# Kernel tuning notes

Hardware: AMD Instinct MI355X
Metric: run time of the kernel (lower is better)

The kernel has to match this reference:

```python
import jax, jax.numpy as jnp
import numpy as np

B, T, D_MODEL, D_FF, NUM_EXPERTS, TOP_K = 8, 4096, 512, 2048, 8, 2
VOCAB = 50257


def setup_inputs() -> dict:
    key = jax.random.key(0)
    k_x, k_id, k_w1, k_w2 = jax.random.split(key, 4)
    x = jax.random.normal(k_x, (B, T, D_MODEL), dtype=jnp.float32)
    token_ids = jax.random.randint(k_id, (B, T), 0, VOCAB, dtype=jnp.int32)
    # stacked expert MLP params: Linear(D,F) -> GELU -> Linear(F,D)
    W1 = jax.random.normal(k_w1, (NUM_EXPERTS, D_MODEL, D_FF), dtype=jnp.float32) * 0.02
    b1 = jnp.zeros((NUM_EXPERTS, D_FF), dtype=jnp.float32)
    W2 = jax.random.normal(k_w2, (NUM_EXPERTS, D_FF, D_MODEL), dtype=jnp.float32) * 0.02
    b2 = jnp.zeros((NUM_EXPERTS, D_MODEL), dtype=jnp.float32)
    return {"x": x, "token_ids": token_ids, "W1": W1, "b1": b1, "W2": W2, "b2": b2}


def reference(x, token_ids, W1, b1, W2, b2):
    Bx, Tx, D = x.shape
    E = W1.shape[0]
    top_k = TOP_K
    # hash routing: expert_ids[b,t,k] = (b*T + token_ids[b,t] + k) % E
    rows = (jnp.arange(Bx, dtype=jnp.int32) * Tx)[:, None, None]           # (B,1,1)
    offs = jnp.arange(top_k, dtype=jnp.int32)                               # (K,)
    expert_ids = (rows + token_ids[:, :, None] + offs) % E                  # (B,T,K)
    onehot = jax.nn.one_hot(expert_ids, E, dtype=jnp.float32)               # (B,T,K,E)
    hits = onehot.sum(axis=2)                                               # (B,T,E) hit counts
    # per-hit combine weight in torch source: (1/top_k)/top_k = 1/top_k^2
    comb_w = hits / float(top_k * top_k)
    # masked-dense expert MLP == dense MLP on x with output masked (per-token ops)
    out = jnp.zeros_like(x)
    for e in range(E):  # fixed small loop over experts
        h = jax.nn.gelu(x @ W1[e] + b1[e], approximate=False)               # (B,T,F)
        y = h @ W2[e] + b2[e]                                               # (B,T,D)
        out = out + y * comb_w[..., e:e + 1]
    expert_counts = hits.sum(axis=(0, 1))                                   # (E,)
    return out, expert_ids, expert_counts
```

## Files before the change

### kernel.cpp

```cpp
#include <hip/hip_runtime.h>
#include <math.h>

#define NUM_E 8
#define NTOK  32768
#define TSEQ  4096
#define DM    512
#define DF    2048
#define CAP   6144

typedef unsigned short ushort_t;
typedef __attribute__((ext_vector_type(8))) short short8;
typedef __attribute__((ext_vector_type(4))) float floatx4;

__device__ __forceinline__ unsigned short f2bf(float f){
  union { float f; unsigned int u; } v; v.f = f;
  unsigned int u = v.u;
  unsigned int r = (u + 0x7FFFu + ((u >> 16) & 1u)) >> 16;
  return (unsigned short)r;
}

__device__ __forceinline__ float gelu_fast(float h){
  float z = h * (1.5957691216057308f + 0.0713548162726009f * h * h);
  float e = __expf(-z);
  return h * __builtin_amdgcn_rcpf(1.0f + e);
}

__device__ __forceinline__ void gld_lds16(const void* g, void* l){
  __builtin_amdgcn_global_load_lds(
      (const __attribute__((address_space(1))) unsigned int*)g,
      (__attribute__((address_space(3))) unsigned int*)l, 16, 0, 0);
}

__global__ void k_init(int* cnt){
  if (threadIdx.x < NUM_E) cnt[threadIdx.x] = 0;
}

__global__ __launch_bounds__(1024) void k_route(
    const int* __restrict__ tok, float* __restrict__ ids_out,
    int* __restrict__ cnt, int* __restrict__ list){
  __shared__ int lcnt[NUM_E];
  __shared__ int lbase[NUM_E];
  int tid = threadIdx.x;
  if (tid < NUM_E) lcnt[tid] = 0;
  __syncthreads();
  int flat = blockIdx.x * 1024 + tid;
  int b = flat >> 12;
  int t = tok[flat];
  int base = b * TSEQ + t;
  int e0 = base & 7;
  int e1 = (base + 1) & 7;
  ids_out[2*flat]   = (float)e0;
  ids_out[2*flat+1] = (float)e1;
  int lpos = atomicAdd(&lcnt[e0], 1);
  __syncthreads();
  if (tid < NUM_E) lbase[tid] = atomicAdd(&cnt[tid], lcnt[tid]);
  __syncthreads();
  int pos = lbase[e0] + lpos;
  if (pos < CAP) list[e0*CAP + pos] = flat;
}

__global__ void k_finalize(const int* __restrict__ cnt, int* __restrict__ off,
                           float* __restrict__ counts_out){
  int tid = threadIdx.x;
  if (tid == 0){
    int s = 0;
    for (int c = 0; c < NUM_E; c++){ off[c] = s; s += cnt[c]; }
    off[NUM_E] = s;
  }
  if (tid < NUM_E)
    counts_out[tid] = (float)(cnt[tid] + cnt[(tid + 7) & 7]);
}

__global__ void k_convert_x(const float* __restrict__ x, ushort_t* __restrict__ xb){
  int i = blockIdx.x * blockDim.x + threadIdx.x;
  float4 v = ((const float4*)x)[i];
  ushort4 o;
  o.x = f2bf(v.x); o.y = f2bf(v.y); o.z = f2bf(v.z); o.w = f2bf(v.w);
  ((ushort4*)xb)[i] = o;
}

__global__ void k_transpose_cvt(const float* __restrict__ in, ushort_t* __restrict__ out,
                                int R, int C){
  __shared__ ushort_t s[64][65];
  int e = blockIdx.z;
  int c0 = blockIdx.x * 64, r0 = blockIdx.y * 64;
  const float* ine = in + (size_t)e * R * C;
  ushort_t* oute = out + (size_t)e * R * C;
  int tx = threadIdx.x & 63, ty = threadIdx.x >> 6;
  for (int rr = ty; rr < 64; rr += 4)
    s[rr][tx] = f2bf(ine[(size_t)(r0+rr)*C + c0 + tx]);
  __syncthreads();
  for (int cc = ty; cc < 64; cc += 4)
    oute[(size_t)(c0+cc)*R + r0 + tx] = s[tx][cc];
}


__global__ __launch_bounds__(256, 4) void k_gemm1(
    const ushort_t* __restrict__ xb, const ushort_t* __restrict__ w1t,
    const float* __restrict__ b1,
    const int* __restrict__ cnt, const int* __restrict__ off,
    const int* __restrict__ list, ushort_t* __restrict__ H, int c0)
{
  int c = c0 + (blockIdx.z >> 1), slot = blockIdx.z & 1;
  int e = (c + slot) & 7;
  int n_c = cnt[c];
  int m0 = blockIdx.x * 128;
  if (m0 >= n_c) return;
  int n0 = blockIdx.y * 128;

  __shared__ alignas(16) ushort_t As[128*64];
  __shared__ alignas(16) ushort_t Bs[128*64];
  __shared__ unsigned int rowoff[128];

  int tid = threadIdx.x;
  int lane = tid & 63, w = tid >> 6;

  if (tid < 128){
    int i = m0 + tid;
    int tk = list[c*CAP + ((i < n_c) ? i : 0)];
    rowoff[tid] = (unsigned int)tk * (DM*2);
  }
  __syncthreads();

  int rl = lane >> 3;
  int cc = (lane & 7) ^ rl;
  unsigned int aoff[4], boff[4];
  const char* w1te = (const char*)w1t + (size_t)e * ((size_t)DF*DM*2);
  #pragma unroll
  for (int j = 0; j < 4; j++){
    int r = j*32 + w*8 + rl;
    aoff[j] = rowoff[r] + (unsigned int)cc*16u;
    boff[j] = (unsigned int)(n0 + r) * (DM*2) + (unsigned int)cc*16u;
  }

  floatx4 acc[4][4];
  #pragma unroll
  for (int a = 0; a < 4; a++)
    #pragma unroll
    for (int q = 0; q < 4; q++) acc[a][q] = floatx4{0.f,0.f,0.f,0.f};

  int wr = w >> 1, wc = w & 1;
  int col = lane & 15, quad = lane >> 4;
  int xa = col & 7;
  const ushort_t* A0 = As + (wr*64 + col)*64 + (quad ^ xa)*8;
  const ushort_t* A1 = As + (wr*64 + col)*64 + ((quad + 4) ^ xa)*8;
  const ushort_t* B0 = Bs + (wc*64 + col)*64 + (quad ^ xa)*8;
  const ushort_t* B1 = Bs + (wc*64 + col)*64 + ((quad + 4) ^ xa)*8;
  char* AsW = (char*)As + w*1024;
  char* BsW = (char*)Bs + w*1024;

  for (int k0 = 0; k0 < DM; k0 += 64){
    #pragma unroll
    for (int j = 0; j < 4; j++){
      gld_lds16((const char*)xb + aoff[j] + k0*2, AsW + j*4096);
      gld_lds16(w1te + boff[j] + k0*2, BsW + j*4096);
    }
    __syncthreads();
    {
      short8 a[4], bfr[4];
      #pragma unroll
      for (int mi = 0; mi < 4; mi++) a[mi] = *(const short8*)(A0 + mi*1024);
      #pragma unroll
      for (int ni = 0; ni < 4; ni++) bfr[ni] = *(const short8*)(B0 + ni*1024);
      #pragma unroll
      for (int mi = 0; mi < 4; mi++)
        #pragma unroll
        for (int ni = 0; ni < 4; ni++)
          acc[mi][ni] = __builtin_amdgcn_mfma_f32_16x16x32_bf16(a[mi], bfr[ni], acc[mi][ni], 0, 0, 0);
      #pragma unroll
      for (int mi = 0; mi < 4; mi++) a[mi] = *(const short8*)(A1 + mi*1024);
      #pragma unroll
      for (int ni = 0; ni < 4; ni++) bfr[ni] = *(const short8*)(B1 + ni*1024);
      #pragma unroll
      for (int mi = 0; mi < 4; mi++)
        #pragma unroll
        for (int ni = 0; ni < 4; ni++)
          acc[mi][ni] = __builtin_amdgcn_mfma_f32_16x16x32_bf16(a[mi], bfr[ni], acc[mi][ni], 0, 0, 0);
    }
    __syncthreads();
  }

  int hbase = off[c] - off[c0];
  const float* b1e = b1 + e*DF;
  #pragma unroll
  for (int mi = 0; mi < 4; mi++){
    #pragma unroll
    for (int r = 0; r < 4; r++){
      int m = wr*64 + mi*16 + quad*4 + r;
      int i = m0 + m;
      if (i < n_c){
        size_t hrow = (size_t)(hbase + i)*(2*DF) + (size_t)slot*DF + n0 + wc*64;
        #pragma unroll
        for (int ni = 0; ni < 4; ni++){
          int nl = ni*16 + col;
          float v = acc[mi][ni][r] + b1e[n0 + wc*64 + nl];
          H[hrow + nl] = f2bf(gelu_fast(v));
        }
      }
    }
  }
}

__global__ __launch_bounds__(256, 4) void k_gemm2(
    const ushort_t* __restrict__ H, const ushort_t* __restrict__ w2t,
    const float* __restrict__ b2,
    const int* __restrict__ cnt, const int* __restrict__ off,
    const int* __restrict__ list, float* __restrict__ out, int c0, int nb)
{
  int c = c0 + blockIdx.z;
  int e1 = (c + 1) & 7;
  int n_c = cnt[c];
  int m0 = blockIdx.x * 128;
  if (m0 >= n_c) return;
  int n0 = blockIdx.y * 128;

  __shared__ alignas(16) ushort_t As[128*64];
  __shared__ alignas(16) ushort_t Bs[128*64];
  __shared__ int rowtok[128];

  int tid = threadIdx.x;
  int lane = tid & 63, w = tid >> 6;
  int rowbase = off[c] - off[c0];
  int phaseTok = off[c0 + nb] - off[c0];

  if (tid < 128){
    int i = m0 + tid;
    rowtok[tid] = list[c*CAP + ((i < n_c) ? i : 0)];
  }

  int rl = lane >> 3;
  int cc = (lane & 7) ^ rl;
  unsigned int aoff[4], boff[4];
  #pragma unroll
  for (int j = 0; j < 4; j++){
    int r = j*32 + w*8 + rl;
    int rg = rowbase + m0 + r;
    if (rg > phaseTok - 1) rg = phaseTok - 1;
    aoff[j] = (unsigned int)rg * (2*DF*2) + (unsigned int)cc*16u;
    boff[j] = (unsigned int)(n0 + r) * (DF*2) + (unsigned int)cc*16u;
  }
  const char* bb0 = (const char*)w2t + (size_t)c  * ((size_t)DM*DF*2);
  const char* bb1 = (const char*)w2t + (size_t)e1 * ((size_t)DM*DF*2);

  floatx4 acc[4][4];
  #pragma unroll
  for (int a = 0; a < 4; a++)
    #pragma unroll
    for (int q = 0; q < 4; q++) acc[a][q] = floatx4{0.f,0.f,0.f,0.f};

  int wr = w >> 1, wc = w & 1;
  int col = lane & 15, quad = lane >> 4;
  int xa = col & 7;
  const ushort_t* A0 = As + (wr*64 + col)*64 + (quad ^ xa)*8;
  const ushort_t* A1 = As + (wr*64 + col)*64 + ((quad + 4) ^ xa)*8;
  const ushort_t* B0 = Bs + (wc*64 + col)*64 + (quad ^ xa)*8;
  const ushort_t* B1 = Bs + (wc*64 + col)*64 + ((quad + 4) ^ xa)*8;
  char* AsW = (char*)As + w*1024;
  char* BsW = (char*)Bs + w*1024;

  for (int k0 = 0; k0 < 2*DF; k0 += 64){
    const char* bb = (k0 < DF) ? (bb0 + k0*2) : (bb1 + (k0 - DF)*2);
    #pragma unroll
    for (int j = 0; j < 4; j++){
      gld_lds16((const char*)H + aoff[j] + k0*2, AsW + j*4096);
      gld_lds16(bb + boff[j], BsW + j*4096);
    }
    __syncthreads();
    {
      short8 a[4], bfr[4];
      #pragma unroll
      for (int mi = 0; mi < 4; mi++) a[mi] = *(const short8*)(A0 + mi*1024);
      #pragma unroll
      for (int ni = 0; ni < 4; ni++) bfr[ni] = *(const short8*)(B0 + ni*1024);
      #pragma unroll
      for (int mi = 0; mi < 4; mi++)
        #pragma unroll
        for (int ni = 0; ni < 4; ni++)
          acc[mi][ni] = __builtin_amdgcn_mfma_f32_16x16x32_bf16(a[mi], bfr[ni], acc[mi][ni], 0, 0, 0);
      #pragma unroll
      for (int mi = 0; mi < 4; mi++) a[mi] = *(const short8*)(A1 + mi*1024);
      #pragma unroll
      for (int ni = 0; ni < 4; ni++) bfr[ni] = *(const short8*)(B1 + ni*1024);
      #pragma unroll
      for (int mi = 0; mi < 4; mi++)
        #pragma unroll
        for (int ni = 0; ni < 4; ni++)
          acc[mi][ni] = __builtin_amdgcn_mfma_f32_16x16x32_bf16(a[mi], bfr[ni], acc[mi][ni], 0, 0, 0);
    }
    __syncthreads();
  }

  const float* b2a = b2 + c*DM;
  const float* b2b = b2 + e1*DM;
  #pragma unroll
  for (int mi = 0; mi < 4; mi++){
    #pragma unroll
    for (int r = 0; r < 4; r++){
      int m = wr*64 + mi*16 + quad*4 + r;
      int i = m0 + m;
      if (i < n_c){
        int tk = rowtok[m];
        float* orow = out + (size_t)tk*DM + n0 + wc*64;
        #pragma unroll
        for (int ni = 0; ni < 4; ni++){
          int nl = ni*16 + col;
          int gn = n0 + wc*64 + nl;
          orow[nl] = 0.25f * (acc[mi][ni][r] + b2a[gn] + b2b[gn]);
        }
      }
    }
  }
}

extern "C" void kernel_launch(void* const* d_in, const int* in_sizes, int n_in,
                              void* d_out, int out_size, void* d_ws, size_t ws_size,
                              hipStream_t stream){
  const float* x   = (const float*)d_in[0];
  const int*   tok = (const int*)d_in[1];
  const float* W1  = (const float*)d_in[2];
  const float* b1  = (const float*)d_in[3];
  const float* W2  = (const float*)d_in[4];
  const float* b2  = (const float*)d_in[5];

  float* out        = (float*)d_out;
  float* ids_out    = out + (size_t)NTOK*DM;
  float* counts_out = ids_out + (size_t)NTOK*2;

  char* ws = (char*)d_ws;
  int* cnt  = (int*)ws;
  int* off  = cnt + 16;
  int* list = (int*)(ws + 4096);
  ushort_t* w1t = (ushort_t*)(ws + (1 << 20));
  ushort_t* w2t = w1t + (size_t)NUM_E*DF*DM;
  ushort_t* xb  = w2t + (size_t)NUM_E*DM*DF;
  ushort_t* H   = (ushort_t*)(ws + (65ull << 20));

  size_t fixed_b = 65ull << 20;
  size_t avail = (ws_size > fixed_b) ? (ws_size - fixed_b) : 0;
  int nb = 0;
  for (int cand = 8; cand >= 1; cand >>= 1){
    size_t need = ((size_t)cand * 4096 + 1024) * (size_t)(2*DF) * 2;
    if (need <= avail){ nb = cand; break; }
  }
  if (nb == 0) nb = 1;

  k_init<<<1, 64, 0, stream>>>(cnt);
  k_route<<<NTOK/1024, 1024, 0, stream>>>(tok, ids_out, cnt, list);
  k_finalize<<<1, 64, 0, stream>>>(cnt, off, counts_out);
  k_convert_x<<<(NTOK*DM/4)/256, 256, 0, stream>>>(x, xb);
  k_transpose_cvt<<<dim3(DF/64, DM/64, NUM_E), 256, 0, stream>>>(W1, w1t, DM, DF);
  k_transpose_cvt<<<dim3(DM/64, DF/64, NUM_E), 256, 0, stream>>>(W2, w2t, DF, DM);

  for (int c0 = 0; c0 < NUM_E; c0 += nb){
    k_gemm1<<<dim3(CAP/128, DF/128, 2*nb), 256, 0, stream>>>(
        xb, w1t, b1, cnt, off, list, H, c0);
    k_gemm2<<<dim3(CAP/128, DM/128, nb), 256, 0, stream>>>(
        H, w2t, b2, cnt, off, list, out, c0, nb);
  }
}
```

Measured before the change: 581.8 us.

## Triple-buffer LDS pipeline with 256x128 tiles and 512-thread blocks in both GEMMs

Result: slower. 742.9 us (+27.7%).

```diff
diff --git a/kernel.cpp b/kernel.cpp
--- a/kernel.cpp
+++ b/kernel.cpp
@@ -11,6 +11,9 @@
 typedef unsigned short ushort_t;
 typedef __attribute__((ext_vector_type(8))) short short8;
 typedef __attribute__((ext_vector_type(4))) float floatx4;
+
+#define WAITVM(N) asm volatile("s_waitcnt vmcnt(" #N ")" ::: "memory")
+#define BARv()    asm volatile("s_barrier" ::: "memory")
 
 __device__ __forceinline__ unsigned short f2bf(float f){
   union { float f; unsigned int u; } v; v.f = f;
@@ -95,7 +98,7 @@
 }
 
 
-__global__ __launch_bounds__(256, 4) void k_gemm1(
+__global__ __launch_bounds__(512, 2) void k_gemm1(
     const ushort_t* __restrict__ xb, const ushort_t* __restrict__ w1t,
     const float* __restrict__ b1,
     const int* __restrict__ cnt, const int* __restrict__ off,
@@ -104,18 +107,19 @@
   int c = c0 + (blockIdx.z >> 1), slot = blockIdx.z & 1;
   int e = (c + slot) & 7;
   int n_c = cnt[c];
-  int m0 = blockIdx.x * 128;
+  int m0 = blockIdx.x * 256;
   if (m0 >= n_c) return;
   int n0 = blockIdx.y * 128;
 
-  __shared__ alignas(16) ushort_t As[128*64];
-  __shared__ alignas(16) ushort_t Bs[128*64];
-  __shared__ unsigned int rowoff[128];
+  extern __shared__ char smem[];
+  char* AsB = smem;
+  char* BsB = smem + 98304;
+  __shared__ unsigned int rowoff[256];
 
   int tid = threadIdx.x;
   int lane = tid & 63, w = tid >> 6;
 
-  if (tid < 128){
+  if (tid < 256){
     int i = m0 + tid;
     int tk = list[c*CAP + ((i < n_c) ? i : 0)];
     rowoff[tid] = (unsigned int)tk * (DM*2);
@@ -124,14 +128,15 @@
 
   int rl = lane >> 3;
   int cc = (lane & 7) ^ rl;
-  unsigned int aoff[4], boff[4];
+  unsigned int aoff[4], boff[2];
+  const char* xc = (const char*)xb;
   const char* w1te = (const char*)w1t + (size_t)e * ((size_t)DF*DM*2);
   #pragma unroll
-  for (int j = 0; j < 4; j++){
-    int r = j*32 + w*8 + rl;
-    aoff[j] = rowoff[r] + (unsigned int)cc*16u;
-    boff[j] = (unsigned int)(n0 + r) * (DM*2) + (unsigned int)cc*16u;
-  }
+  for (int u = 0; u < 4; u++)
+    aoff[u] = rowoff[u*64 + w*8 + rl] + (unsigned int)cc*16u;
+  #pragma unroll
+  for (int u = 0; u < 2; u++)
+    boff[u] = (unsigned int)(n0 + u*64 + w*8 + rl) * (DM*2) + (unsigned int)cc*16u;
 
   floatx4 acc[4][4];
   #pragma unroll
@@ -142,43 +147,56 @@
   int wr = w >> 1, wc = w & 1;
   int col = lane & 15, quad = lane >> 4;
   int xa = col & 7;
-  const ushort_t* A0 = As + (wr*64 + col)*64 + (quad ^ xa)*8;
-  const ushort_t* A1 = As + (wr*64 + col)*64 + ((quad + 4) ^ xa)*8;
-  const ushort_t* B0 = Bs + (wc*64 + col)*64 + (quad ^ xa)*8;
-  const ushort_t* B1 = Bs + (wc*64 + col)*64 + ((quad + 4) ^ xa)*8;
-  char* AsW = (char*)As + w*1024;
-  char* BsW = (char*)Bs + w*1024;
-
-  for (int k0 = 0; k0 < DM; k0 += 64){
-    #pragma unroll
-    for (int j = 0; j < 4; j++){
-      gld_lds16((const char*)xb + aoff[j] + k0*2, AsW + j*4096);
-      gld_lds16(w1te + boff[j] + k0*2, BsW + j*4096);
+  int ar0 = (wr*64 + col)*128 + ((quad    ) ^ xa)*16;
+  int ar1 = (wr*64 + col)*128 + ((quad + 4) ^ xa)*16;
+  int br0 = (wc*64 + col)*128 + ((quad    ) ^ xa)*16;
+  int br1 = (wc*64 + col)*128 + ((quad + 4) ^ xa)*16;
+  char* adstw = AsB + w*1024;
+  char* bdstw = BsB + w*1024;
+
+#define STG1(tt, sb) do{                                      \
+    unsigned int kk2 = (unsigned int)(tt)*128u;               \
+    char* ad = adstw + (sb)*32768;                            \
+    char* bd = bdstw + (sb)*16384;                            \
+    gld_lds16(xc + (aoff[0] + kk2), ad);                      \
+    gld_lds16(xc + (aoff[1] + kk2), ad + 8192);               \
+    gld_lds16(xc + (aoff[2] + kk2), ad + 16384);              \
+    gld_lds16(xc + (aoff[3] + kk2), ad + 24576);              \
+    gld_lds16(w1te + (boff[0] + kk2), bd);                    \
+    gld_lds16(w1te + (boff[1] + kk2), bd + 8192);             \
+  }while(0)
+
+  STG1(0, 0);
+  STG1(1, 1);
+  int sl = 0;
+  #pragma unroll 1
+  for (int t = 0; t < 8; t++){
+    if (t + 2 < 8){ int sb = sl + 2; if (sb >= 3) sb -= 3; STG1(t+2, sb); }
+    if (t < 6) WAITVM(12); else if (t == 6) WAITVM(6); else WAITVM(0);
+    BARv();
+    const char* Aslot = AsB + sl*32768;
+    const char* Bslot = BsB + sl*16384;
+    short8 av0[4], av1[4], bv0[4], bv1[4];
+    #pragma unroll
+    for (int i2 = 0; i2 < 4; i2++){
+      av0[i2] = *(const short8*)(Aslot + ar0 + i2*2048);
+      av1[i2] = *(const short8*)(Aslot + ar1 + i2*2048);
+      bv0[i2] = *(const short8*)(Bslot + br0 + i2*2048);
+      bv1[i2] = *(const short8*)(Bslot + br1 + i2*2048);
     }
-    __syncthreads();
-    {
-      short8 a[4], bfr[4];
+    __builtin_amdgcn_s_setprio(1);
+    #pragma unroll
+    for (int mi = 0; mi < 4; mi++)
       #pragma unroll
-      for (int mi = 0; mi < 4; mi++) a[mi] = *(const short8*)(A0 + mi*1024);
-      #pragma unroll
-      for (int ni = 0; ni < 4; ni++) bfr[ni] = *(const short8*)(B0 + ni*1024);
-      #pragma unroll
-      for (int mi = 0; mi < 4; mi++)
-        #pragma unroll
-        for (int ni = 0; ni < 4; ni++)
-          acc[mi][ni] = __builtin_amdgcn_mfma_f32_16x16x32_bf16(a[mi], bfr[ni], acc[mi][ni], 0, 0, 0);
-      #pragma unroll
-      for (int mi = 0; mi < 4; mi++) a[mi] = *(const short8*)(A1 + mi*1024);
-      #pragma unroll
-      for (int ni = 0; ni < 4; ni++) bfr[ni] = *(const short8*)(B1 + ni*1024);
-      #pragma unroll
-      for (int mi = 0; mi < 4; mi++)
-        #pragma unroll
-        for (int ni = 0; ni < 4; ni++)
-          acc[mi][ni] = __builtin_amdgcn_mfma_f32_16x16x32_bf16(a[mi], bfr[ni], acc[mi][ni], 0, 0, 0);
-    }
-    __syncthreads();
-  }
+      for (int ni = 0; ni < 4; ni++){
+        acc[mi][ni] = __builtin_amdgcn_mfma_f32_16x16x32_bf16(av0[mi], bv0[ni], acc[mi][ni], 0, 0, 0);
+        acc[mi][ni] = __builtin_amdgcn_mfma_f32_16x16x32_bf16(av1[mi], bv1[ni], acc[mi][ni], 0, 0, 0);
+      }
+    __builtin_amdgcn_s_setprio(0);
+    BARv();
+    sl++; if (sl == 3) sl = 0;
+  }
+#undef STG1
 
   int hbase = off[c] - off[c0];
   const float* b1e = b1 + e*DF;
@@ -201,7 +219,7 @@
   }
 }
 
-__global__ __launch_bounds__(256, 4) void k_gemm2(
+__global__ __launch_bounds__(512, 2) void k_gemm2(
     const ushort_t* __restrict__ H, const ushort_t* __restrict__ w2t,
     const float* __restrict__ b2,
     const int* __restrict__ cnt, const int* __restrict__ off,
@@ -210,35 +228,40 @@
   int c = c0 + blockIdx.z;
   int e1 = (c + 1) & 7;
   int n_c = cnt[c];
-  int m0 = blockIdx.x * 128;
+  int m0 = blockIdx.x * 256;
   if (m0 >= n_c) return;
   int n0 = blockIdx.y * 128;
 
-  __shared__ alignas(16) ushort_t As[128*64];
-  __shared__ alignas(16) ushort_t Bs[128*64];
-  __shared__ int rowtok[128];
+  extern __shared__ char smem[];
+  char* AsB = smem;
+  char* BsB = smem + 98304;
+  __shared__ int rowtok[256];
 
   int tid = threadIdx.x;
   int lane = tid & 63, w = tid >> 6;
   int rowbase = off[c] - off[c0];
   int phaseTok = off[c0 + nb] - off[c0];
 
-  if (tid < 128){
+  if (tid < 256){
     int i = m0 + tid;
     rowtok[tid] = list[c*CAP + ((i < n_c) ? i : 0)];
   }
+  __syncthreads();
 
   int rl = lane >> 3;
   int cc = (lane & 7) ^ rl;
-  unsigned int aoff[4], boff[4];
-  #pragma unroll
-  for (int j = 0; j < 4; j++){
-    int r = j*32 + w*8 + rl;
-    int rg = rowbase + m0 + r;
+  unsigned int aoff[4], boff[2];
+  #pragma unroll
+  for (int u = 0; u < 4; u++){
+    int rg = rowbase + m0 + u*64 + w*8 + rl;
     if (rg > phaseTok - 1) rg = phaseTok - 1;
-    aoff[j] = (unsigned int)rg * (2*DF*2) + (unsigned int)cc*16u;
-    boff[j] = (unsigned int)(n0 + r) * (DF*2) + (unsigned int)cc*16u;
-  }
+    aoff[u] = (unsigned int)rg * (2*DF*2) + (unsigned int)cc*16u;
+  }
+  #pragma unroll
+  for (int u = 0; u < 2; u++)
+    boff[u] = (unsigned int)(n0 + u*64 + w*8 + rl) * (DF*2) + (unsigned int)cc*16u;
+
+  const char* Hc  = (const char*)H;
   const char* bb0 = (const char*)w2t + (size_t)c  * ((size_t)DM*DF*2);
   const char* bb1 = (const char*)w2t + (size_t)e1 * ((size_t)DM*DF*2);
 
@@ -251,44 +274,57 @@
   int wr = w >> 1, wc = w & 1;
   int col = lane & 15, quad = lane >> 4;
   int xa = col & 7;
-  const ushort_t* A0 = As + (wr*64 + col)*64 + (quad ^ xa)*8;
-  const ushort_t* A1 = As + (wr*64 + col)*64 + ((quad + 4) ^ xa)*8;
-  const ushort_t* B0 = Bs + (wc*64 + col)*64 + (quad ^ xa)*8;
-  const ushort_t* B1 = Bs + (wc*64 + col)*64 + ((quad + 4) ^ xa)*8;
-  char* AsW = (char*)As + w*1024;
-  char* BsW = (char*)Bs + w*1024;
-
-  for (int k0 = 0; k0 < 2*DF; k0 += 64){
-    const char* bb = (k0 < DF) ? (bb0 + k0*2) : (bb1 + (k0 - DF)*2);
-    #pragma unroll
-    for (int j = 0; j < 4; j++){
-      gld_lds16((const char*)H + aoff[j] + k0*2, AsW + j*4096);
-      gld_lds16(bb + boff[j], BsW + j*4096);
+  int ar0 = (wr*64 + col)*128 + ((quad    ) ^ xa)*16;
+  int ar1 = (wr*64 + col)*128 + ((quad + 4) ^ xa)*16;
+  int br0 = (wc*64 + col)*128 + ((quad    ) ^ xa)*16;
+  int br1 = (wc*64 + col)*128 + ((quad + 4) ^ xa)*16;
+  char* adstw = AsB + w*1024;
+  char* bdstw = BsB + w*1024;
+
+#define STG2(tt, sb) do{                                                   \
+    unsigned int kk2 = (unsigned int)(tt)*128u;                            \
+    const char* bsrc = ((tt) < 32) ? (bb0 + kk2) : (bb1 + (kk2 - 4096u)); \
+    char* ad = adstw + (sb)*32768;                                         \
+    char* bd = bdstw + (sb)*16384;                                         \
+    gld_lds16(Hc + (aoff[0] + kk2), ad);                                   \
+    gld_lds16(Hc + (aoff[1] + kk2), ad + 8192);                            \
+    gld_lds16(Hc + (aoff[2] + kk2), ad + 16384);                           \
+    gld_lds16(Hc + (aoff[3] + kk2), ad + 24576);                           \
+    gld_lds16(bsrc + boff[0], bd);                                         \
+    gld_lds16(bsrc + boff[1], bd + 8192);                                  \
+  }while(0)
+
+  STG2(0, 0);
+  STG2(1, 1);
+  int sl = 0;
+  #pragma unroll 1
+  for (int t = 0; t < 64; t++){
+    if (t + 2 < 64){ int sb = sl + 2; if (sb >= 3) sb -= 3; STG2(t+2, sb); }
+    if (t < 62) WAITVM(12); else if (t == 62) WAITVM(6); else WAITVM(0);
+    BARv();
+    const char* Aslot = AsB + sl*32768;
+    const char* Bslot = BsB + sl*16384;
+    short8 av0[4], av1[4], bv0[4], bv1[4];
+    #pragma unroll
+    for (int i2 = 0; i2 < 4; i2++){
+      av0[i2] = *(const short8*)(Aslot + ar0 + i2*2048);
+      av1[i2] = *(const short8*)(Aslot + ar1 + i2*2048);
+      bv0[i2] = *(const short8*)(Bslot + br0 + i2*2048);
+      bv1[i2] = *(const short8*)(Bslot + br1 + i2*2048);
     }
-    __syncthreads();
-    {
-      short8 a[4], bfr[4];
+    __builtin_amdgcn_s_setprio(1);
+    #pragma unroll
+    for (int mi = 0; mi < 4; mi++)
       #pragma unroll
-      for (int mi = 0; mi < 4; mi++) a[mi] = *(const short8*)(A0 + mi*1024);
-      #pragma unroll
-      for (int ni = 0; ni < 4; ni++) bfr[ni] = *(const short8*)(B0 + ni*1024);
-      #pragma unroll
-      for (int mi = 0; mi < 4; mi++)
-        #pragma unroll
-        for (int ni = 0; ni < 4; ni++)
-          acc[mi][ni] = __builtin_amdgcn_mfma_f32_16x16x32_bf16(a[mi], bfr[ni], acc[mi][ni], 0, 0, 0);
-      #pragma unroll
-      for (int mi = 0; mi < 4; mi++) a[mi] = *(const short8*)(A1 + mi*1024);
-      #pragma unroll
-      for (int ni = 0; ni < 4; ni++) bfr[ni] = *(const short8*)(B1 + ni*1024);
-      #pragma unroll
-      for (int mi = 0; mi < 4; mi++)
-        #pragma unroll
-        for (int ni = 0; ni < 4; ni++)
-          acc[mi][ni] = __builtin_amdgcn_mfma_f32_16x16x32_bf16(a[mi], bfr[ni], acc[mi][ni], 0, 0, 0);
-    }
-    __syncthreads();
-  }
+      for (int ni = 0; ni < 4; ni++){
+        acc[mi][ni] = __builtin_amdgcn_mfma_f32_16x16x32_bf16(av0[mi], bv0[ni], acc[mi][ni], 0, 0, 0);
+        acc[mi][ni] = __builtin_amdgcn_mfma_f32_16x16x32_bf16(av1[mi], bv1[ni], acc[mi][ni], 0, 0, 0);
+      }
+    __builtin_amdgcn_s_setprio(0);
+    BARv();
+    sl++; if (sl == 3) sl = 0;
+  }
+#undef STG2
 
   const float* b2a = b2 + c*DM;
   const float* b2b = b2 + e1*DM;
@@ -335,6 +371,15 @@
   ushort_t* xb  = w2t + (size_t)NUM_E*DM*DF;
   ushort_t* H   = (ushort_t*)(ws + (65ull << 20));
 
+  static int attr_done = 0;
+  if (!attr_done){
+    hipFuncSetAttribute((const void*)k_gemm1,
+                        hipFuncAttributeMaxDynamicSharedMemorySize, 147456);
+    hipFuncSetAttribute((const void*)k_gemm2,
+                        hipFuncAttributeMaxDynamicSharedMemorySize, 147456);
+    attr_done = 1;
+  }
+
   size_t fixed_b = 65ull << 20;
   size_t avail = (ws_size > fixed_b) ? (ws_size - fixed_b) : 0;
   int nb = 0;
@@ -352,9 +397,9 @@
   k_transpose_cvt<<<dim3(DM/64, DF/64, NUM_E), 256, 0, stream>>>(W2, w2t, DF, DM);
 
   for (int c0 = 0; c0 < NUM_E; c0 += nb){
-    k_gemm1<<<dim3(CAP/128, DF/128, 2*nb), 256, 0, stream>>>(
+    k_gemm1<<<dim3(CAP/256, DF/128, 2*nb), 512, 147456, stream>>>(
         xb, w1t, b1, cnt, off, list, H, c0);
-    k_gemm2<<<dim3(CAP/128, DM/128, nb), 256, 0, stream>>>(
+    k_gemm2<<<dim3(CAP/256, DM/128, nb), 512, 147456, stream>>>(
         H, w2t, b2, cnt, off, list, out, c0, nb);
   }
 }
```

## Enlarge gemm1 tile to 256x256 with double-buffered LDS and interleaved loads

Applied to the files above, without the earlier changes.

After: 617.7 us. 1.06x slower.

```diff
diff --git a/kernel.cpp b/kernel.cpp
--- a/kernel.cpp
+++ b/kernel.cpp
@@ -11,6 +11,9 @@
 typedef unsigned short ushort_t;
 typedef __attribute__((ext_vector_type(8))) short short8;
 typedef __attribute__((ext_vector_type(4))) float floatx4;
+
+#define WAITVM(N) asm volatile("s_waitcnt vmcnt(" #N ")" ::: "memory")
+#define BARv()    asm volatile("s_barrier" ::: "memory")
 
 __device__ __forceinline__ unsigned short f2bf(float f){
   union { float f; unsigned int u; } v; v.f = f;
@@ -94,8 +97,7 @@
     oute[(size_t)(c0+cc)*R + r0 + tx] = s[tx][cc];
 }
 
-
-__global__ __launch_bounds__(256, 4) void k_gemm1(
+__global__ __launch_bounds__(512, 2) void k_gemm1(
     const ushort_t* __restrict__ xb, const ushort_t* __restrict__ w1t,
     const float* __restrict__ b1,
     const int* __restrict__ cnt, const int* __restrict__ off,
@@ -104,18 +106,17 @@
   int c = c0 + (blockIdx.z >> 1), slot = blockIdx.z & 1;
   int e = (c + slot) & 7;
   int n_c = cnt[c];
-  int m0 = blockIdx.x * 128;
+  int m0 = blockIdx.x * 256;
   if (m0 >= n_c) return;
-  int n0 = blockIdx.y * 128;
-
-  __shared__ alignas(16) ushort_t As[128*64];
-  __shared__ alignas(16) ushort_t Bs[128*64];
-  __shared__ unsigned int rowoff[128];
+  int n0 = blockIdx.y * 256;
+
+  extern __shared__ char smem[];
+  __shared__ unsigned int rowoff[256];
 
   int tid = threadIdx.x;
   int lane = tid & 63, w = tid >> 6;
 
-  if (tid < 128){
+  if (tid < 256){
     int i = m0 + tid;
     int tk = list[c*CAP + ((i < n_c) ? i : 0)];
     rowoff[tid] = (unsigned int)tk * (DM*2);
@@ -125,68 +126,98 @@
   int rl = lane >> 3;
   int cc = (lane & 7) ^ rl;
   unsigned int aoff[4], boff[4];
+  const char* xc = (const char*)xb;
   const char* w1te = (const char*)w1t + (size_t)e * ((size_t)DF*DM*2);
   #pragma unroll
   for (int j = 0; j < 4; j++){
-    int r = j*32 + w*8 + rl;
+    int r = j*64 + w*8 + rl;
     aoff[j] = rowoff[r] + (unsigned int)cc*16u;
     boff[j] = (unsigned int)(n0 + r) * (DM*2) + (unsigned int)cc*16u;
   }
 
-  floatx4 acc[4][4];
-  #pragma unroll
-  for (int a = 0; a < 4; a++)
+  floatx4 acc[8][4];
+  #pragma unroll
+  for (int a = 0; a < 8; a++)
     #pragma unroll
     for (int q = 0; q < 4; q++) acc[a][q] = floatx4{0.f,0.f,0.f,0.f};
 
-  int wr = w >> 1, wc = w & 1;
+  int wr = w >> 2, wc = w & 3;
   int col = lane & 15, quad = lane >> 4;
   int xa = col & 7;
-  const ushort_t* A0 = As + (wr*64 + col)*64 + (quad ^ xa)*8;
-  const ushort_t* A1 = As + (wr*64 + col)*64 + ((quad + 4) ^ xa)*8;
-  const ushort_t* B0 = Bs + (wc*64 + col)*64 + (quad ^ xa)*8;
-  const ushort_t* B1 = Bs + (wc*64 + col)*64 + ((quad + 4) ^ xa)*8;
-  char* AsW = (char*)As + w*1024;
-  char* BsW = (char*)Bs + w*1024;
-
-  for (int k0 = 0; k0 < DM; k0 += 64){
-    #pragma unroll
-    for (int j = 0; j < 4; j++){
-      gld_lds16((const char*)xb + aoff[j] + k0*2, AsW + j*4096);
-      gld_lds16(w1te + boff[j] + k0*2, BsW + j*4096);
-    }
-    __syncthreads();
-    {
-      short8 a[4], bfr[4];
-      #pragma unroll
-      for (int mi = 0; mi < 4; mi++) a[mi] = *(const short8*)(A0 + mi*1024);
-      #pragma unroll
-      for (int ni = 0; ni < 4; ni++) bfr[ni] = *(const short8*)(B0 + ni*1024);
-      #pragma unroll
-      for (int mi = 0; mi < 4; mi++)
-        #pragma unroll
-        for (int ni = 0; ni < 4; ni++)
-          acc[mi][ni] = __builtin_amdgcn_mfma_f32_16x16x32_bf16(a[mi], bfr[ni], acc[mi][ni], 0, 0, 0);
-      #pragma unroll
-      for (int mi = 0; mi < 4; mi++) a[mi] = *(const short8*)(A1 + mi*1024);
-      #pragma unroll
-      for (int ni = 0; ni < 4; ni++) bfr[ni] = *(const short8*)(B1 + ni*1024);
-      #pragma unroll
-      for (int mi = 0; mi < 4; mi++)
-        #pragma unroll
-        for (int ni = 0; ni < 4; ni++)
-          acc[mi][ni] = __builtin_amdgcn_mfma_f32_16x16x32_bf16(a[mi], bfr[ni], acc[mi][ni], 0, 0, 0);
-    }
-    __syncthreads();
-  }
+  int qx0 = ((quad    ) ^ xa)*16;
+  int qx1 = ((quad + 4) ^ xa)*16;
+  int arow = (wr*128 + col)*128;
+  int brow = (wc*64  + col)*128;
+
+#define STG_B(tt, J0, J1) do{                                        \
+    char* bd = smem + 65536 + ((tt)&1)*32768 + w*1024;               \
+    gld_lds16(w1te + (boff[J0] + (unsigned int)(tt)*128u), bd + (J0)*8192); \
+    gld_lds16(w1te + (boff[J1] + (unsigned int)(tt)*128u), bd + (J1)*8192); \
+  }while(0)
+#define STG_A(tt, J0, J1) do{                                        \
+    char* ad = smem + ((tt)&1)*32768 + w*1024;                       \
+    gld_lds16(xc + (aoff[J0] + (unsigned int)(tt)*128u), ad + (J0)*8192); \
+    gld_lds16(xc + (aoff[J1] + (unsigned int)(tt)*128u), ad + (J1)*8192); \
+  }while(0)
+
+#define MFMA_PAIR(MI) do{                                            \
+    short8 a00 = *(const short8*)(Ab + arow + (MI)*2048   + qx0);    \
+    short8 a01 = *(const short8*)(Ab + arow + (MI)*2048   + qx1);    \
+    short8 a10 = *(const short8*)(Ab + arow + (MI+1)*2048 + qx0);    \
+    short8 a11 = *(const short8*)(Ab + arow + (MI+1)*2048 + qx1);    \
+    __builtin_amdgcn_s_setprio(1);                                   \
+    _Pragma("unroll")                                                \
+    for (int ni = 0; ni < 4; ni++){                                  \
+      acc[MI][ni]   = __builtin_amdgcn_mfma_f32_16x16x32_bf16(a00, bfr[ni][0], acc[MI][ni],   0,0,0); \
+      acc[MI][ni]   = __builtin_amdgcn_mfma_f32_16x16x32_bf16(a01, bfr[ni][1], acc[MI][ni],   0,0,0); \
+      acc[MI+1][ni] = __builtin_amdgcn_mfma_f32_16x16x32_bf16(a10, bfr[ni][0], acc[MI+1][ni], 0,0,0); \
+      acc[MI+1][ni] = __builtin_amdgcn_mfma_f32_16x16x32_bf16(a11, bfr[ni][1], acc[MI+1][ni], 0,0,0); \
+    }                                                                \
+    __builtin_amdgcn_s_setprio(0);                                   \
+  }while(0)
+
+  STG_B(0, 0, 1); STG_B(0, 2, 3);
+  STG_A(0, 0, 1); STG_A(0, 2, 3);
+
+  #pragma unroll 1
+  for (int t = 0; t < 8; t++){
+    const char* Ab = smem + (t&1)*32768;
+    const char* Bb = smem + 65536 + (t&1)*32768;
+    int t1 = t + 1;
+    if (t1 < 8){ STG_B(t1, 0, 1); WAITVM(2); } else { WAITVM(0); }
+    BARv();
+    short8 bfr[4][2];
+    #pragma unroll
+    for (int ni = 0; ni < 4; ni++){
+      bfr[ni][0] = *(const short8*)(Bb + brow + ni*2048 + qx0);
+      bfr[ni][1] = *(const short8*)(Bb + brow + ni*2048 + qx1);
+    }
+    MFMA_PAIR(0);
+    BARv();
+    if (t1 < 8) STG_B(t1, 2, 3);
+    BARv();
+    MFMA_PAIR(2);
+    BARv();
+    if (t1 < 8) STG_A(t1, 0, 1);
+    BARv();
+    MFMA_PAIR(4);
+    BARv();
+    if (t1 < 8) STG_A(t1, 2, 3);
+    BARv();
+    MFMA_PAIR(6);
+    BARv();
+  }
+#undef STG_A
+#undef STG_B
+#undef MFMA_PAIR
 
   int hbase = off[c] - off[c0];
   const float* b1e = b1 + e*DF;
   #pragma unroll
-  for (int mi = 0; mi < 4; mi++){
+  for (int mi = 0; mi < 8; mi++){
     #pragma unroll
     for (int r = 0; r < 4; r++){
-      int m = wr*64 + mi*16 + quad*4 + r;
+      int m = wr*128 + mi*16 + quad*4 + r;
       int i = m0 + m;
       if (i < n_c){
         size_t hrow = (size_t)(hbase + i)*(2*DF) + (size_t)slot*DF + n0 + wc*64;
@@ -335,6 +366,13 @@
   ushort_t* xb  = w2t + (size_t)NUM_E*DM*DF;
   ushort_t* H   = (ushort_t*)(ws + (65ull << 20));
 
+  static int attr_done = 0;
+  if (!attr_done){
+    hipFuncSetAttribute((const void*)k_gemm1,
+                        hipFuncAttributeMaxDynamicSharedMemorySize, 131072);
+    attr_done = 1;
+  }
+
   size_t fixed_b = 65ull << 20;
   size_t avail = (ws_size > fixed_b) ? (ws_size - fixed_b) : 0;
   int nb = 0;
@@ -352,7 +390,7 @@
   k_transpose_cvt<<<dim3(DM/64, DF/64, NUM_E), 256, 0, stream>>>(W2, w2t, DF, DM);
 
   for (int c0 = 0; c0 < NUM_E; c0 += nb){
-    k_gemm1<<<dim3(CAP/128, DF/128, 2*nb), 256, 0, stream>>>(
+    k_gemm1<<<dim3(CAP/256, DF/256, 2*nb), 512, 131072, stream>>>(
         xb, w1t, b1, cnt, off, list, H, c0);
     k_gemm2<<<dim3(CAP/128, DM/128, nb), 256, 0, stream>>>(
         H, w2t, b2, cnt, off, list, out, c0, nb);
```
